# Kernel optimization log

Hardware: AMD Instinct MI355X
Metric: run time of the kernel (lower is better)

The kernel has to match this reference:

```python
import jax, jax.numpy as jnp
import numpy as np

HEAD_COUNT = 6  # module scales by head_count**-0.5, not head_size
SCALE = HEAD_COUNT ** (-0.5)


def setup_inputs() -> dict:
    key = jax.random.key(0)
    kx, kq, kk, kv = jax.random.split(key, 4)
    B, T, C, H = 512, 128, 384, 64
    x = jax.random.normal(kx, (B, T, C), dtype=jnp.float32)
    init = (1.0 / np.sqrt(C)).astype(np.float32)
    Wq = jax.random.normal(kq, (C, H), dtype=jnp.float32) * init
    Wk = jax.random.normal(kk, (C, H), dtype=jnp.float32) * init
    Wv = jax.random.normal(kv, (C, H), dtype=jnp.float32) * init
    return {"x": x, "Wq": Wq, "Wk": Wk, "Wv": Wv}


def reference(x, Wq, Wk, Wv):
    # x: [B, T, C]; Wq/Wk/Wv: [C, H]
    q = jnp.einsum('btc,ch->bth', x, Wq)
    k = jnp.einsum('btc,ch->bth', x, Wk)
    v = jnp.einsum('btc,ch->bth', x, Wv)
    # scores: [B, T, T], scaled by head_count**-0.5 (faithful to source)
    scores = jnp.einsum('bth,bsh->bts', q, k) * SCALE
    T = x.shape[1]
    causal = jnp.tril(jnp.ones((T, T), dtype=bool))
    scores = jnp.where(causal, scores, -jnp.inf)
    weights = jax.nn.softmax(scores, axis=-1)
    # dropout omitted (eval mode / identity for reference baseline)
    return jnp.einsum('bts,bsh->bth', weights, v)
```

## Files before the change

### kernel.cpp

```cpp
#include <hip/hip_runtime.h>
#include <hip/hip_bf16.h>


#define B_ 512
#define T_ 128
#define C_ 384
#define H_ 64

typedef __bf16 bf16;
typedef __attribute__((ext_vector_type(8))) __bf16 bf16x8;
typedef __attribute__((ext_vector_type(4))) __bf16 bf16x4;
typedef __attribute__((ext_vector_type(4))) float f32x4;

__global__ void build_wt(const float* __restrict__ Wq, const float* __restrict__ Wk,
                         const float* __restrict__ Wv, bf16* __restrict__ Wt)
{
    int t = blockIdx.x * 256 + threadIdx.x;
    if (t >= 12 * 12 * 64) return;
    int lane = t & 63;
    int tn   = (t >> 6) % 12;
    int kc   = t / (12 * 64);
    int lm = lane & 15, quad = lane >> 4;
    int n = tn * 16 + lm;
    int j = n >> 6, h = n & 63;
    const float* Wp = (j == 0) ? Wq : (j == 1) ? Wk : Wv;
    int k0 = kc * 32 + quad * 8;
    bf16x8 v;
#pragma unroll
    for (int e = 0; e < 8; ++e) v[e] = (bf16)Wp[(k0 + e) * H_ + h];
    *(bf16x8*)&Wt[t * 8] = v;
}


__launch_bounds__(256, 2)
__global__ void head_fused(const float* __restrict__ x,
                           const bf16* __restrict__ Wt,
                           float* __restrict__ out)
{
    __shared__ bf16 lds[24576];
    bf16* Qs  = lds;
    bf16* Ks  = lds + 8192;
    bf16* Vts = lds + 16384;
    bf16* Ps  = lds;

    const int tid  = threadIdx.x;
    const int w    = tid >> 6;
    const int lane = tid & 63;
    const int lm   = lane & 15;
    const int quad = lane >> 4;
    const int b    = blockIdx.x;

    const float* xb = x + (size_t)b * (T_ * C_);

    f32x4 acc[2][12];
#pragma unroll
    for (int i = 0; i < 2; ++i)
#pragma unroll
        for (int t = 0; t < 12; ++t) acc[i][t] = (f32x4){0.f, 0.f, 0.f, 0.f};

    const float* xr0 = xb + (32 * w + lm) * C_ + quad * 8;
    const float* xr1 = xb + (32 * w + 16 + lm) * C_ + quad * 8;
    const bf16*  wl  = Wt + lane * 8;

    float4 xA[4], xB[4];

    auto LD = [&](int kc, float4* xr) {
        xr[0] = *(const float4*)(xr0 + kc * 32);
        xr[1] = *(const float4*)(xr0 + kc * 32 + 4);
        xr[2] = *(const float4*)(xr1 + kc * 32);
        xr[3] = *(const float4*)(xr1 + kc * 32 + 4);
    };
    auto CHUNK = [&](int kc, const float4* xr) {
        bf16x8 a0 = {(bf16)xr[0].x, (bf16)xr[0].y, (bf16)xr[0].z, (bf16)xr[0].w,
                     (bf16)xr[1].x, (bf16)xr[1].y, (bf16)xr[1].z, (bf16)xr[1].w};
        bf16x8 a1 = {(bf16)xr[2].x, (bf16)xr[2].y, (bf16)xr[2].z, (bf16)xr[2].w,
                     (bf16)xr[3].x, (bf16)xr[3].y, (bf16)xr[3].z, (bf16)xr[3].w};
        const bf16* wp = wl + kc * 6144;
#pragma unroll
        for (int tn = 0; tn < 12; ++tn) {
            bf16x8 bfr = *(const bf16x8*)(wp + tn * 512);
            acc[0][tn] = __builtin_amdgcn_mfma_f32_16x16x32_bf16(a0, bfr, acc[0][tn], 0, 0, 0);
            acc[1][tn] = __builtin_amdgcn_mfma_f32_16x16x32_bf16(a1, bfr, acc[1][tn], 0, 0, 0);
        }
    };

    LD(0, xA);
#pragma unroll
    for (int kc = 0; kc < 12; kc += 2) {
        LD(kc + 1, xB);
        CHUNK(kc, xA);
        if (kc + 2 < 12) LD(kc + 2, xA);
        CHUNK(kc + 1, xB);
    }

#pragma unroll
    for (int i = 0; i < 2; ++i) {
#pragma unroll
        for (int tn = 0; tn < 12; ++tn) {
            int gn = 16 * tn + lm;
            int j = gn >> 6, h = gn & 63;
            int m0 = 32 * w + 16 * i + quad * 4;
            if (j == 2) {
                bf16x4 v4 = {(bf16)acc[i][tn][0], (bf16)acc[i][tn][1],
                             (bf16)acc[i][tn][2], (bf16)acc[i][tn][3]};
                int pc = (m0 & 7) | ((((m0 >> 3) ^ (h & 15)) & 15) << 3);
                *(bf16x4*)&Vts[h * 128 + pc] = v4;
            } else {
                bf16* dst = (j == 0) ? Qs : Ks;
#pragma unroll
                for (int r = 0; r < 4; ++r) {
                    int m = m0 + r;
                    int pc = (h & 7) | ((((h >> 3) ^ (m & 7)) & 7) << 3);
                    dst[m * 64 + pc] = (bf16)acc[i][tn][r];
                }
            }
        }
    }
    __syncthreads();

    const float SCALE = 0.40824829046386307f;
    const int tmg0 = w, tmg1 = 7 - w;

    f32x4 sacc[2][8];
#pragma unroll
    for (int i = 0; i < 2; ++i)
#pragma unroll
        for (int t = 0; t < 8; ++t) sacc[i][t] = (f32x4){0.f, 0.f, 0.f, 0.f};

#pragma unroll
    for (int i = 0; i < 2; ++i) {
        const int tm = i ? tmg1 : tmg0;
        const int mrow = 16 * tm + lm;
        bf16x8 qa[2];
#pragma unroll
        for (int ks = 0; ks < 2; ++ks) {
            int phys = ((ks * 4 + quad) ^ (mrow & 7)) & 7;
            qa[ks] = *(const bf16x8*)&Qs[mrow * 64 + phys * 8];
        }
#pragma unroll
        for (int tn = 0; tn < 8; ++tn) {
            if (tn <= tm) {
                int nrow = 16 * tn + lm;
#pragma unroll
                for (int ks = 0; ks < 2; ++ks) {
                    int phys = ((ks * 4 + quad) ^ (nrow & 7)) & 7;
                    bf16x8 kb = *(const bf16x8*)&Ks[nrow * 64 + phys * 8];
                    sacc[i][tn] =
                        __builtin_amdgcn_mfma_f32_16x16x32_bf16(qa[ks], kb, sacc[i][tn], 0, 0, 0);
                }
            }
        }
    }

#pragma unroll
    for (int i = 0; i < 2; ++i) {
        const int tm = i ? tmg1 : tmg0;
#pragma unroll
        for (int r = 0; r < 4; ++r) {
            int m = 16 * tm + quad * 4 + r;
            float mx = -1e30f;
#pragma unroll
            for (int tn = 0; tn < 8; ++tn) {
                if (tn <= tm) {
                    int n = 16 * tn + lm;
                    float v = (n <= m) ? sacc[i][tn][r] * SCALE : -1e30f;
                    sacc[i][tn][r] = v;
                    mx = fmaxf(mx, v);
                }
            }
#pragma unroll
            for (int off = 1; off < 16; off <<= 1) mx = fmaxf(mx, __shfl_xor(mx, off, 16));
            float sum = 0.f;
#pragma unroll
            for (int tn = 0; tn < 8; ++tn) {
                if (tn <= tm) {
                    float e = __expf(sacc[i][tn][r] - mx);
                    sacc[i][tn][r] = e;
                    sum += e;
                }
            }
#pragma unroll
            for (int off = 1; off < 16; off <<= 1) sum += __shfl_xor(sum, off, 16);
            float inv = 1.f / sum;
#pragma unroll
            for (int tn = 0; tn < 8; ++tn) {
                if (tn <= tm) sacc[i][tn][r] *= inv;
            }
        }
    }

    __syncthreads();

#pragma unroll
    for (int i = 0; i < 2; ++i) {
        const int tm = i ? tmg1 : tmg0;
#pragma unroll
        for (int tn = 0; tn < 8; ++tn) {
            if (tn <= tm) {
                int n = 16 * tn + lm;
#pragma unroll
                for (int r = 0; r < 4; ++r) {
                    int m = 16 * tm + quad * 4 + r;
                    int pc = (n & 7) | ((((n >> 3) ^ (m & 15)) & 15) << 3);
                    Ps[m * 128 + pc] = (bf16)sacc[i][tn][r];
                }
            }
        }
        if ((tm & 1) == 0) {
            int m = 16 * tm + lm;
            int c0 = 16 * (tm + 1) + quad * 4;
            int pc = (c0 & 7) | ((((c0 >> 3) ^ (m & 15)) & 15) << 3);
            *(bf16x4*)&Ps[m * 128 + pc] =
                (bf16x4){(bf16)0.f, (bf16)0.f, (bf16)0.f, (bf16)0.f};
        }
    }

    f32x4 oacc[2][4];
#pragma unroll
    for (int i = 0; i < 2; ++i)
#pragma unroll
        for (int t = 0; t < 4; ++t) oacc[i][t] = (f32x4){0.f, 0.f, 0.f, 0.f};

#pragma unroll
    for (int i = 0; i < 2; ++i) {
        const int tm = i ? tmg1 : tmg0;
        const int mrow = 16 * tm + lm;
        const int nks = (tm + 2) >> 1;
        for (int ks = 0; ks < nks; ++ks) {
            int unit = ks * 4 + quad;
            int phys = (unit ^ (mrow & 15)) & 15;
            bf16x8 pa = *(const bf16x8*)&Ps[mrow * 128 + phys * 8];
#pragma unroll
            for (int th = 0; th < 4; ++th) {
                int hrow = 16 * th + lm;
                int ph2 = (unit ^ (hrow & 15)) & 15;
                bf16x8 vb = *(const bf16x8*)&Vts[hrow * 128 + ph2 * 8];
                oacc[i][th] =
                    __builtin_amdgcn_mfma_f32_16x16x32_bf16(pa, vb, oacc[i][th], 0, 0, 0);
            }
        }
    }

    float* ob = out + (size_t)b * (T_ * H_);
#pragma unroll
    for (int i = 0; i < 2; ++i) {
        const int tm = i ? tmg1 : tmg0;
#pragma unroll
        for (int th = 0; th < 4; ++th) {
            int h = 16 * th + lm;
#pragma unroll
            for (int r = 0; r < 4; ++r) {
                int m = 16 * tm + quad * 4 + r;
                ob[m * 64 + h] = oacc[i][th][r];
            }
        }
    }
}

extern "C" void kernel_launch(void* const* d_in, const int* in_sizes, int n_in,
                              void* d_out, int out_size, void* d_ws, size_t ws_size,
                              hipStream_t stream) {
    const float* x  = (const float*)d_in[0];
    const float* Wq = (const float*)d_in[1];
    const float* Wk = (const float*)d_in[2];
    const float* Wv = (const float*)d_in[3];
    float* o = (float*)d_out;
    bf16* Wt = (bf16*)d_ws;
    build_wt<<<dim3(36), dim3(256), 0, stream>>>(Wq, Wk, Wv, Wt);
    head_fused<<<dim3(B_), dim3(256), 0, stream>>>(x, Wt, o);
}
```

Baseline: 185.8 us.

## Double block to 512 threads with 2x4 warp grid for QKV projection

Launches 8 waves per block instead of 4. The projection GEMM is retiled so each wave owns a 64-row by 48-column tile (two row groups by four column groups), which reuses each x fragment across three weight fragments. The attention phase is reassigned to one 16-row query tile per wave instead of two balanced tiles. This aims for more wave-level parallelism and fewer redundant x loads per block, at the cost of causal load imbalance across waves and a tighter register budget under the new launch bounds.

Measured after the change: 191.0 us. 2.8% more time.

```diff
diff --git a/kernel.cpp b/kernel.cpp
--- a/kernel.cpp
+++ b/kernel.cpp
@@ -32,7 +32,7 @@
 }
 
 
-__launch_bounds__(256, 2)
+__launch_bounds__(512, 4)
 __global__ void head_fused(const float* __restrict__ x,
                            const bf16* __restrict__ Wt,
                            float* __restrict__ out)
@@ -48,61 +48,63 @@
     const int lane = tid & 63;
     const int lm   = lane & 15;
     const int quad = lane >> 4;
+    const int mg   = w >> 2;
+    const int ng   = w & 3;
     const int b    = blockIdx.x;
 
     const float* xb = x + (size_t)b * (T_ * C_);
 
-    f32x4 acc[2][12];
-#pragma unroll
-    for (int i = 0; i < 2; ++i)
-#pragma unroll
-        for (int t = 0; t < 12; ++t) acc[i][t] = (f32x4){0.f, 0.f, 0.f, 0.f};
-
-    const float* xr0 = xb + (32 * w + lm) * C_ + quad * 8;
-    const float* xr1 = xb + (32 * w + 16 + lm) * C_ + quad * 8;
-    const bf16*  wl  = Wt + lane * 8;
-
-    float4 xA[4], xB[4];
-
-    auto LD = [&](int kc, float4* xr) {
-        xr[0] = *(const float4*)(xr0 + kc * 32);
-        xr[1] = *(const float4*)(xr0 + kc * 32 + 4);
-        xr[2] = *(const float4*)(xr1 + kc * 32);
-        xr[3] = *(const float4*)(xr1 + kc * 32 + 4);
+    f32x4 acc[4][3];
+#pragma unroll
+    for (int mf = 0; mf < 4; ++mf)
+#pragma unroll
+        for (int nf = 0; nf < 3; ++nf) acc[mf][nf] = (f32x4){0.f, 0.f, 0.f, 0.f};
+
+    const float* xr   = xb + (size_t)(64 * mg + lm) * C_ + quad * 8;
+    const bf16*  wbase = Wt + (size_t)(3 * ng) * 512 + lane * 8;
+
+    float4 buf[8];
+    auto LD = [&](int kc) {
+#pragma unroll
+        for (int mf = 0; mf < 4; ++mf) {
+            const float4* p = (const float4*)(xr + mf * 16 * C_ + kc * 32);
+            buf[2 * mf]     = p[0];
+            buf[2 * mf + 1] = p[1];
+        }
     };
-    auto CHUNK = [&](int kc, const float4* xr) {
-        bf16x8 a0 = {(bf16)xr[0].x, (bf16)xr[0].y, (bf16)xr[0].z, (bf16)xr[0].w,
-                     (bf16)xr[1].x, (bf16)xr[1].y, (bf16)xr[1].z, (bf16)xr[1].w};
-        bf16x8 a1 = {(bf16)xr[2].x, (bf16)xr[2].y, (bf16)xr[2].z, (bf16)xr[2].w,
-                     (bf16)xr[3].x, (bf16)xr[3].y, (bf16)xr[3].z, (bf16)xr[3].w};
-        const bf16* wp = wl + kc * 6144;
-#pragma unroll
-        for (int tn = 0; tn < 12; ++tn) {
-            bf16x8 bfr = *(const bf16x8*)(wp + tn * 512);
-            acc[0][tn] = __builtin_amdgcn_mfma_f32_16x16x32_bf16(a0, bfr, acc[0][tn], 0, 0, 0);
-            acc[1][tn] = __builtin_amdgcn_mfma_f32_16x16x32_bf16(a1, bfr, acc[1][tn], 0, 0, 0);
-        }
-    };
-
-    LD(0, xA);
-#pragma unroll
-    for (int kc = 0; kc < 12; kc += 2) {
-        LD(kc + 1, xB);
-        CHUNK(kc, xA);
-        if (kc + 2 < 12) LD(kc + 2, xA);
-        CHUNK(kc + 1, xB);
-    }
-
-#pragma unroll
-    for (int i = 0; i < 2; ++i) {
-#pragma unroll
-        for (int tn = 0; tn < 12; ++tn) {
+
+    LD(0);
+#pragma unroll
+    for (int kc = 0; kc < 12; ++kc) {
+        bf16x8 afr[4];
+#pragma unroll
+        for (int mf = 0; mf < 4; ++mf) {
+            float4 p0 = buf[2 * mf], p1 = buf[2 * mf + 1];
+            afr[mf] = (bf16x8){(bf16)p0.x, (bf16)p0.y, (bf16)p0.z, (bf16)p0.w,
+                               (bf16)p1.x, (bf16)p1.y, (bf16)p1.z, (bf16)p1.w};
+        }
+        if (kc < 11) LD(kc + 1);
+#pragma unroll
+        for (int nf = 0; nf < 3; ++nf) {
+            bf16x8 bfr = *(const bf16x8*)(wbase + (size_t)kc * 6144 + nf * 512);
+#pragma unroll
+            for (int mf = 0; mf < 4; ++mf)
+                acc[mf][nf] =
+                    __builtin_amdgcn_mfma_f32_16x16x32_bf16(afr[mf], bfr, acc[mf][nf], 0, 0, 0);
+        }
+    }
+
+#pragma unroll
+    for (int mf = 0; mf < 4; ++mf) {
+#pragma unroll
+        for (int nf = 0; nf < 3; ++nf) {
+            int tn = 3 * ng + nf;
             int gn = 16 * tn + lm;
             int j = gn >> 6, h = gn & 63;
-            int m0 = 32 * w + 16 * i + quad * 4;
+            int m0 = 64 * mg + 16 * mf + quad * 4;
             if (j == 2) {
-                bf16x4 v4 = {(bf16)acc[i][tn][0], (bf16)acc[i][tn][1],
-                             (bf16)acc[i][tn][2], (bf16)acc[i][tn][3]};
+                bf16x4 v4 = {(bf16)acc[mf][nf][0], (bf16)acc[mf][nf][1],
+                             (bf16)acc[mf][nf][2], (bf16)acc[mf][nf][3]};
                 int pc = (m0 & 7) | ((((m0 >> 3) ^ (h & 15)) & 15) << 3);
                 *(bf16x4*)&Vts[h * 128 + pc] = v4;
             } else {
@@ -111,7 +113,7 @@
                 for (int r = 0; r < 4; ++r) {
                     int m = m0 + r;
                     int pc = (h & 7) | ((((h >> 3) ^ (m & 7)) & 7) << 3);
-                    dst[m * 64 + pc] = (bf16)acc[i][tn][r];
+                    dst[m * 64 + pc] = (bf16)acc[mf][nf][r];
                 }
             }
         }
@@ -119,140 +121,115 @@
     __syncthreads();
 
     const float SCALE = 0.40824829046386307f;
-    const int tmg0 = w, tmg1 = 7 - w;
-
-    f32x4 sacc[2][8];
-#pragma unroll
-    for (int i = 0; i < 2; ++i)
-#pragma unroll
-        for (int t = 0; t < 8; ++t) sacc[i][t] = (f32x4){0.f, 0.f, 0.f, 0.f};
-
-#pragma unroll
-    for (int i = 0; i < 2; ++i) {
-        const int tm = i ? tmg1 : tmg0;
-        const int mrow = 16 * tm + lm;
-        bf16x8 qa[2];
-#pragma unroll
-        for (int ks = 0; ks < 2; ++ks) {
-            int phys = ((ks * 4 + quad) ^ (mrow & 7)) & 7;
-            qa[ks] = *(const bf16x8*)&Qs[mrow * 64 + phys * 8];
-        }
-#pragma unroll
-        for (int tn = 0; tn < 8; ++tn) {
-            if (tn <= tm) {
-                int nrow = 16 * tn + lm;
-#pragma unroll
-                for (int ks = 0; ks < 2; ++ks) {
-                    int phys = ((ks * 4 + quad) ^ (nrow & 7)) & 7;
-                    bf16x8 kb = *(const bf16x8*)&Ks[nrow * 64 + phys * 8];
-                    sacc[i][tn] =
-                        __builtin_amdgcn_mfma_f32_16x16x32_bf16(qa[ks], kb, sacc[i][tn], 0, 0, 0);
-                }
-            }
-        }
-    }
-
-#pragma unroll
-    for (int i = 0; i < 2; ++i) {
-        const int tm = i ? tmg1 : tmg0;
-#pragma unroll
-        for (int r = 0; r < 4; ++r) {
-            int m = 16 * tm + quad * 4 + r;
-            float mx = -1e30f;
-#pragma unroll
-            for (int tn = 0; tn < 8; ++tn) {
-                if (tn <= tm) {
-                    int n = 16 * tn + lm;
-                    float v = (n <= m) ? sacc[i][tn][r] * SCALE : -1e30f;
-                    sacc[i][tn][r] = v;
-                    mx = fmaxf(mx, v);
-                }
-            }
-#pragma unroll
-            for (int off = 1; off < 16; off <<= 1) mx = fmaxf(mx, __shfl_xor(mx, off, 16));
-            float sum = 0.f;
-#pragma unroll
-            for (int tn = 0; tn < 8; ++tn) {
-                if (tn <= tm) {
-                    float e = __expf(sacc[i][tn][r] - mx);
-                    sacc[i][tn][r] = e;
-                    sum += e;
-                }
-            }
-#pragma unroll
-            for (int off = 1; off < 16; off <<= 1) sum += __shfl_xor(sum, off, 16);
-            float inv = 1.f / sum;
-#pragma unroll
-            for (int tn = 0; tn < 8; ++tn) {
-                if (tn <= tm) sacc[i][tn][r] *= inv;
-            }
-        }
-    }
-
-    __syncthreads();
-
-#pragma unroll
-    for (int i = 0; i < 2; ++i) {
-        const int tm = i ? tmg1 : tmg0;
+    const int tm = w;
+    const int mrow = 16 * tm + lm;
+
+    f32x4 sacc[8];
+#pragma unroll
+    for (int t = 0; t < 8; ++t) sacc[t] = (f32x4){0.f, 0.f, 0.f, 0.f};
+
+    bf16x8 qa[2];
+#pragma unroll
+    for (int ks = 0; ks < 2; ++ks) {
+        int phys = ((ks * 4 + quad) ^ (mrow & 7)) & 7;
+        qa[ks] = *(const bf16x8*)&Qs[mrow * 64 + phys * 8];
+    }
+#pragma unroll
+    for (int tn = 0; tn < 8; ++tn) {
+        if (tn <= tm) {
+            int nrow = 16 * tn + lm;
+#pragma unroll
+            for (int ks = 0; ks < 2; ++ks) {
+                int phys = ((ks * 4 + quad) ^ (nrow & 7)) & 7;
+                bf16x8 kb = *(const bf16x8*)&Ks[nrow * 64 + phys * 8];
+                sacc[tn] =
+                    __builtin_amdgcn_mfma_f32_16x16x32_bf16(qa[ks], kb, sacc[tn], 0, 0, 0);
+            }
+        }
+    }
+
+#pragma unroll
+    for (int r = 0; r < 4; ++r) {
+        int m = 16 * tm + quad * 4 + r;
+        float mx = -1e30f;
 #pragma unroll
         for (int tn = 0; tn < 8; ++tn) {
             if (tn <= tm) {
                 int n = 16 * tn + lm;
-#pragma unroll
-                for (int r = 0; r < 4; ++r) {
-                    int m = 16 * tm + quad * 4 + r;
-                    int pc = (n & 7) | ((((n >> 3) ^ (m & 15)) & 15) << 3);
-                    Ps[m * 128 + pc] = (bf16)sacc[i][tn][r];
-                }
-            }
-        }
-        if ((tm & 1) == 0) {
-            int m = 16 * tm + lm;
-            int c0 = 16 * (tm + 1) + quad * 4;
-            int pc = (c0 & 7) | ((((c0 >> 3) ^ (m & 15)) & 15) << 3);
-            *(bf16x4*)&Ps[m * 128 + pc] =
-                (bf16x4){(bf16)0.f, (bf16)0.f, (bf16)0.f, (bf16)0.f};
-        }
-    }
-
-    f32x4 oacc[2][4];
-#pragma unroll
-    for (int i = 0; i < 2; ++i)
-#pragma unroll
-        for (int t = 0; t < 4; ++t) oacc[i][t] = (f32x4){0.f, 0.f, 0.f, 0.f};
-
-#pragma unroll
-    for (int i = 0; i < 2; ++i) {
-        const int tm = i ? tmg1 : tmg0;
-        const int mrow = 16 * tm + lm;
-        const int nks = (tm + 2) >> 1;
-        for (int ks = 0; ks < nks; ++ks) {
-            int unit = ks * 4 + quad;
-            int phys = (unit ^ (mrow & 15)) & 15;
-            bf16x8 pa = *(const bf16x8*)&Ps[mrow * 128 + phys * 8];
-#pragma unroll
-            for (int th = 0; th < 4; ++th) {
-                int hrow = 16 * th + lm;
-                int ph2 = (unit ^ (hrow & 15)) & 15;
-                bf16x8 vb = *(const bf16x8*)&Vts[hrow * 128 + ph2 * 8];
-                oacc[i][th] =
-                    __builtin_amdgcn_mfma_f32_16x16x32_bf16(pa, vb, oacc[i][th], 0, 0, 0);
-            }
-        }
-    }
-
-    float* ob = out + (size_t)b * (T_ * H_);
-#pragma unroll
-    for (int i = 0; i < 2; ++i) {
-        const int tm = i ? tmg1 : tmg0;
-#pragma unroll
-        for (int th = 0; th < 4; ++th) {
-            int h = 16 * th + lm;
+                float v = (n <= m) ? sacc[tn][r] * SCALE : -1e30f;
+                sacc[tn][r] = v;
+                mx = fmaxf(mx, v);
+            }
+        }
+#pragma unroll
+        for (int off = 1; off < 16; off <<= 1) mx = fmaxf(mx, __shfl_xor(mx, off, 16));
+        float sum = 0.f;
+#pragma unroll
+        for (int tn = 0; tn < 8; ++tn) {
+            if (tn <= tm) {
+                float e = __expf(sacc[tn][r] - mx);
+                sacc[tn][r] = e;
+                sum += e;
+            }
+        }
+#pragma unroll
+        for (int off = 1; off < 16; off <<= 1) sum += __shfl_xor(sum, off, 16);
+        float inv = 1.f / sum;
+#pragma unroll
+        for (int tn = 0; tn < 8; ++tn) {
+            if (tn <= tm) sacc[tn][r] *= inv;
+        }
+    }
+
+    __syncthreads();
+
+#pragma unroll
+    for (int tn = 0; tn < 8; ++tn) {
+        if (tn <= tm) {
+            int n = 16 * tn + lm;
 #pragma unroll
             for (int r = 0; r < 4; ++r) {
                 int m = 16 * tm + quad * 4 + r;
-                ob[m * 64 + h] = oacc[i][th][r];
-            }
+                int pc = (n & 7) | ((((n >> 3) ^ (m & 15)) & 15) << 3);
+                Ps[m * 128 + pc] = (bf16)sacc[tn][r];
+            }
+        }
+    }
+    if ((tm & 1) == 0) {
+        int m = 16 * tm + lm;
+        int c0 = 16 * (tm + 1) + quad * 4;
+        int pc = (c0 & 7) | ((((c0 >> 3) ^ (m & 15)) & 15) << 3);
+        *(bf16x4*)&Ps[m * 128 + pc] =
+            (bf16x4){(bf16)0.f, (bf16)0.f, (bf16)0.f, (bf16)0.f};
+    }
+
+    f32x4 oacc[4];
+#pragma unroll
+    for (int t = 0; t < 4; ++t) oacc[t] = (f32x4){0.f, 0.f, 0.f, 0.f};
+
+    const int nks = (tm + 2) >> 1;
+    for (int ks = 0; ks < nks; ++ks) {
+        int unit = ks * 4 + quad;
+        int phys = (unit ^ (mrow & 15)) & 15;
+        bf16x8 pa = *(const bf16x8*)&Ps[mrow * 128 + phys * 8];
+#pragma unroll
+        for (int th = 0; th < 4; ++th) {
+            int hrow = 16 * th + lm;
+            int ph2 = (unit ^ (hrow & 15)) & 15;
+            bf16x8 vb = *(const bf16x8*)&Vts[hrow * 128 + ph2 * 8];
+            oacc[th] =
+                __builtin_amdgcn_mfma_f32_16x16x32_bf16(pa, vb, oacc[th], 0, 0, 0);
+        }
+    }
+
+    float* ob = out + (size_t)b * (T_ * H_);
+#pragma unroll
+    for (int th = 0; th < 4; ++th) {
+        int h = 16 * th + lm;
+#pragma unroll
+        for (int r = 0; r < 4; ++r) {
+            int m = 16 * tm + quad * 4 + r;
+            ob[m * 64 + h] = oacc[th][r];
         }
     }
 }
@@ -267,5 +244,5 @@
     float* o = (float*)d_out;
     bf16* Wt = (bf16*)d_ws;
     build_wt<<<dim3(36), dim3(256), 0, stream>>>(Wq, Wk, Wv, Wt);
-    head_fused<<<dim3(B_), dim3(256), 0, stream>>>(x, Wt, o);
+    head_fused<<<dim3(B_), dim3(512), 0, stream>>>(x, Wt, o);
 }
```
